# Kernel tuning notes

Measured on AMD Instinct MI355X. Metric: run time of the kernel, lower is better.

Reference implementation:

```python
import math
import jax, jax.numpy as jnp
import numpy as np

SEQ_LEN = 4096
PACK_LEN = 64
DIM = 1024
HEADS = 8
BS = 64
HD = DIM // HEADS
NB = SEQ_LEN // BS
PEN = -10000.0


def _slopes(n):
    start = 2.0 ** (-8.0 / n)
    return np.array([start ** (i + 1) for i in range(n)], dtype=np.float32)


def _dist_matrices():
    sl = _slopes(HEADS)
    idx = np.arange(SEQ_LEN, dtype=np.float32)
    D = sl[:, None, None] * np.abs(idx[:, None] - idx[None, :])  # [H,S,S]
    Dp = sl[:, None, None] * np.full((SEQ_LEN, PACK_LEN), float(BS), np.float32)  # [H,S,P]
    return jnp.asarray(D), jnp.asarray(Dp)


def _mb_index():
    # replicate get_middle_band_distances index construction (row counter from 0)
    M = (NB - 3) * BS
    i_vals = np.arange(2 * BS, SEQ_LEN - BS)
    offset = i_vals // BS - 1
    cols = np.concatenate([
        np.broadcast_to(np.arange(BS), (M, BS)),
        offset[:, None] * BS + np.arange(3 * BS)[None, :],
    ], axis=1)  # [M, 4*BS]
    rows = np.arange(M)
    return rows, cols

_MB_ROWS, _MB_COLS = _mb_index()


def _middle_band_D(D):
    return D[:, _MB_ROWS[:, None], _MB_COLS].reshape(HEADS, NB - 3, BS, 4 * BS)


def _heads(t):
    b, s, _ = t.shape
    return t.reshape(b, s, HEADS, HD).transpose(0, 2, 1, 3)


def reference(X, Cp, attention_mask, WQ, bQ, WK, bK, WV, bV):
    b, S, _ = X.shape
    rsq = 1.0 / math.sqrt(HD)
    D, Dp = _dist_matrices()

    q = _heads(X @ WQ + bQ)        # [b,H,S,hd]
    kx = _heads(X @ WK + bK)
    vx = _heads(X @ WV + bV)
    kcp = _heads(Cp @ WK + bK)     # [b,H,P,hd]
    vcp = _heads(Cp @ WV + bV)

    mask_block = attention_mask.reshape(b, NB, BS)
    exp_to = jnp.concatenate([mask_block[:, 1:-2], mask_block[:, 2:-1], mask_block[:, 3:]], axis=2)
    band_mask = jnp.einsum('blq,blk->blqk', mask_block[:, 2:-1], exp_to)[:, None]  # [b,1,L,bs,3bs]
    mask_v = attention_mask.reshape(b, 1, S, 1)

    # packed (Cp) attention path
    a = jnp.einsum('bhqd,bhkd->bhqk', q, kcp) * rsq - Dp[None] + (1.0 - mask_v) * PEN
    a = jax.nn.softmax(a, axis=-1)
    packed = jnp.einsum('bhqk,bhkd->bhqd', a, vcp) * mask_v  # [b,H,S,hd]

    qb = q.reshape(b, HEADS, NB, BS, HD)
    kb = kx.reshape(b, HEADS, NB, BS, HD)
    vb = vx.reshape(b, HEADS, NB, BS, HD)

    # first two rows attend to blocks 0..3
    k4 = kb[:, :, :4].reshape(b, HEADS, 4 * BS, HD)
    v4 = vb[:, :, :4].reshape(b, HEADS, 4 * BS, HD)
    q2 = qb[:, :, :2].reshape(b, HEADS, 2 * BS, HD)
    a1 = (jnp.einsum('bhqd,bhkd->bhqk', q2, k4) * rsq
          - D[:, :2 * BS, :4 * BS][None]
          + (1.0 - mask_v[:, :, :2 * BS, :1]) * PEN)
    a1 = jax.nn.softmax(a1, axis=-1)
    ctx_first = jnp.einsum('bhqk,bhkd->bhqd', a1, v4).reshape(b, HEADS, 2, BS, HD)

    # middle band: global block 0 + 3-block sliding window
    mk = jnp.concatenate([kb[:, :, 1:-2], kb[:, :, 2:-1], kb[:, :, 3:]], axis=3)  # [b,H,L,3bs,hd]
    mv = jnp.concatenate([vb[:, :, 1:-2], vb[:, :, 2:-1], vb[:, :, 3:]], axis=3)
    slid = jnp.einsum('bhlqd,bhlkd->bhlqk', qb[:, :, 2:-1], mk) + (1.0 - band_mask) * PEN
    glob = (jnp.einsum('bhlqd,bhkd->bhlqk', qb[:, :, 2:-1], kb[:, :, 0])
            + (1.0 - mask_block[:, 2:-1, :][..., None]) * PEN)  # torch-style broadcast (b==1)
    ma = jnp.concatenate([glob, slid], axis=-1) * rsq - _middle_band_D(D)[None]
    ma = jax.nn.softmax(ma, axis=-1)
    ctx_mid = (jnp.einsum('bhlqk,bhkd->bhlqd', ma[..., :BS], vb[:, :, 0])
               + jnp.einsum('bhlqk,bhlkd->bhlqd', ma[..., BS:], mv))

    # last row attends to blocks 0, -3, -2, -1 (no extra mask, as in original)
    kl = jnp.concatenate([kb[:, :, 0], kb[:, :, -3], kb[:, :, -2], kb[:, :, -1]], axis=2)
    vl = jnp.concatenate([vb[:, :, 0], vb[:, :, -3], vb[:, :, -2], vb[:, :, -1]], axis=2)
    al = jnp.einsum('bhqd,bhkd->bhqk', qb[:, :, -1], kl) * rsq - D[:, -BS:, -4 * BS:][None]
    al = jax.nn.softmax(al, axis=-1)
    ctx_last = jnp.einsum('bhqk,bhkd->bhqd', al, vl)[:, :, None]

    ctx = jnp.concatenate([ctx_first, ctx_mid, ctx_last], axis=2).reshape(b, HEADS, S, HD)
    # original does a raw view [b,h,S,hd] -> [b,S,h*hd] (no transpose); reshape matches
    Cx = (ctx + packed).reshape(b, S, HEADS * HD) * attention_mask[..., None]
    return Cx


def setup_inputs() -> dict:
    key = jax.random.key(0)
    ks = jax.random.split(key, 6)
    return {
        'X': jax.random.normal(ks[0], (1, SEQ_LEN, DIM), jnp.float32),
        'Cp': jax.random.normal(ks[1], (1, PACK_LEN, DIM), jnp.float32),
        'attention_mask': jnp.ones((1, SEQ_LEN), jnp.float32),
        'WQ': jax.random.normal(ks[2], (DIM, DIM), jnp.float32) * 0.02,
        'bQ': jnp.zeros((DIM,), jnp.float32),
        'WK': jax.random.normal(ks[3], (DIM, DIM), jnp.float32) * 0.02,
        'bK': jnp.zeros((DIM,), jnp.float32),
        'WV': jax.random.normal(ks[4], (DIM, DIM), jnp.float32) * 0.02,
        'bV': jnp.zeros((DIM,), jnp.float32),
    }
```

## Files before the change

### kernel.cpp

```cpp
#include <hip/hip_runtime.h>
#include <hip/hip_bf16.h>

typedef __bf16 bf16;
typedef __attribute__((ext_vector_type(4))) __bf16 bf16x4;
typedef __attribute__((ext_vector_type(8))) __bf16 bf16x8;
typedef __attribute__((ext_vector_type(4))) float f32x4;

#define SEQ   4096
#define DIMN  1024
#define NHEAD 8
#define HD    128
#define MALL  4160
#define PENV  -10000.0f
#define NT    16
#define NCVT  4160

typedef const __attribute__((address_space(1))) void gvoid_t;
typedef __attribute__((address_space(3))) void lvoid_t;

__global__ __launch_bounds__(256) void prep_kernel(
    const float* __restrict__ X, const float* __restrict__ Cp,
    const float* __restrict__ W0, const float* __restrict__ W1, const float* __restrict__ W2,
    bf16* __restrict__ A, bf16* __restrict__ Wt) {
  const int bid = blockIdx.x;
  if (bid < NCVT) {
    size_t base = ((size_t)bid * 256 + threadIdx.x) * 4;
    const float* src = (base < (size_t)SEQ * DIMN) ? (X + base) : (Cp + (base - (size_t)SEQ * DIMN));
    float4 v = *(const float4*)src;
    bf16x4 o;
    o[0] = (bf16)v.x; o[1] = (bf16)v.y; o[2] = (bf16)v.z; o[3] = (bf16)v.w;
    *(bf16x4*)&A[base] = o;
  } else {
    int tid2 = bid - NCVT;
    int z = tid2 >> 8, rem = tid2 & 255;
    int by = rem >> 4, bx = rem & 15;
    const float* W = (z == 0) ? W0 : ((z == 1) ? W1 : W2);
    bf16* dst = Wt + (size_t)z * DIMN * DIMN;
    __shared__ bf16 tile[64][72];
    int k0 = by * 64, n0 = bx * 64;
    int tx = threadIdx.x & 63, ty = threadIdx.x >> 6;
#pragma unroll
    for (int r = ty; r < 64; r += 4)
      tile[tx][r] = (bf16)W[(size_t)(k0 + r) * DIMN + n0 + tx];
    __syncthreads();
#pragma unroll
    for (int r = ty; r < 64; r += 4)
      dst[(size_t)(n0 + r) * DIMN + k0 + tx] = tile[r][tx];
  }
}

__global__ __launch_bounds__(512) void gemm_qkv_kernel(
    const bf16* __restrict__ A, const bf16* __restrict__ Wt,
    const float* __restrict__ bQ, const float* __restrict__ bK, const float* __restrict__ bV,
    bf16* __restrict__ QKV) {
  const int z = blockIdx.z;
  const int M = (z == 0) ? SEQ : MALL;
  const int m0 = blockIdx.y * 256;
  if (m0 >= M) return;
  const int n0 = blockIdx.x * 256;
  const bf16* Wz = Wt + (size_t)z * DIMN * DIMN;
  const float* bias = (z == 0) ? bQ : ((z == 1) ? bK : bV);
  bf16* out = QKV + (size_t)z * MALL * DIMN;

  __shared__ bf16 SMEM[4][256 * 64];
  bf16 (*Ab)[256 * 64] = &SMEM[0];
  bf16 (*Bb)[256 * 64] = &SMEM[2];

  const int t = threadIdx.x;
  const int lane = t & 63, w = t >> 6;
  const int wm = w >> 2, wn = w & 3;
  const int r16 = lane & 15, g4 = lane >> 4;

  f32x4 acc[8][4] = {};

  auto stageA = [&](int k) {
    int b = k & 1;
#pragma unroll
    for (int i = 0; i < 4; ++i) {
      int segBase = i * 512 + w * 64;
      int seg = segBase + lane;
      int row = seg >> 3;
      int cc = (seg & 7) ^ (row & 7);
      int gm = m0 + row; gm = (gm < M) ? gm : (M - 1);
      __builtin_amdgcn_global_load_lds(
          (gvoid_t*)(A + (size_t)gm * DIMN + k * 64 + cc * 8),
          (lvoid_t*)(&Ab[b][segBase * 8]), 16, 0, 0);
    }
  };
  auto stageB = [&](int k) {
    int b = k & 1;
#pragma unroll
    for (int i = 0; i < 4; ++i) {
      int segBase = i * 512 + w * 64;
      int seg = segBase + lane;
      int row = seg >> 3;
      int cc = (seg & 7) ^ (row & 7);
      int gn = n0 + row;
      __builtin_amdgcn_global_load_lds(
          (gvoid_t*)(Wz + (size_t)gn * DIMN + k * 64 + cc * 8),
          (lvoid_t*)(&Bb[b][segBase * 8]), 16, 0, 0);
    }
  };

  auto rdA = [&](const bf16* Ax, int mf, int kk) -> bf16x8 {
    int row = wm * 128 + mf * 16 + r16;
    return *(const bf16x8*)&Ax[row * 64 + (((kk * 4 + g4) ^ (row & 7)) * 8)];
  };
  auto rdB = [&](const bf16* Bx, int nf, int kk) -> bf16x8 {
    int row = wn * 64 + nf * 16 + r16;
    return *(const bf16x8*)&Bx[row * 64 + (((kk * 4 + g4) ^ (row & 7)) * 8)];
  };

  stageA(0); stageB(0);
  asm volatile("s_waitcnt vmcnt(0)" ::: "memory");
  __builtin_amdgcn_s_barrier();

  for (int k = 0; k < NT; ++k) {
    const bf16* Ax = &Ab[k & 1][0];
    const bf16* Bx = &Bb[k & 1][0];
    bf16x8 aL[4], aH[4], bL[4];

#pragma unroll
    for (int mf = 0; mf < 4; ++mf) aL[mf] = rdA(Ax, mf, 0);
#pragma unroll
    for (int nf = 0; nf < 4; ++nf) bL[nf] = rdB(Bx, nf, 0);
#pragma unroll
    for (int mf = 0; mf < 4; ++mf) aH[mf] = rdA(Ax, 4 + mf, 0);
    if (k + 1 < NT) stageA(k + 1);
    __builtin_amdgcn_sched_barrier(0);

    __builtin_amdgcn_s_setprio(1);
#pragma unroll
    for (int mf = 0; mf < 4; ++mf)
#pragma unroll
      for (int nf = 0; nf < 4; ++nf)
        acc[mf][nf] = __builtin_amdgcn_mfma_f32_16x16x32_bf16(aL[mf], bL[nf], acc[mf][nf], 0, 0, 0);
    __builtin_amdgcn_s_setprio(0);

    bf16x8 aL2[4], bL2[4];
#pragma unroll
    for (int mf = 0; mf < 4; ++mf) aL2[mf] = rdA(Ax, mf, 1);
#pragma unroll
    for (int nf = 0; nf < 4; ++nf) bL2[nf] = rdB(Bx, nf, 1);
    if (k + 1 < NT) stageB(k + 1);
    __builtin_amdgcn_sched_barrier(0);

    __builtin_amdgcn_s_setprio(1);
#pragma unroll
    for (int mf = 0; mf < 4; ++mf)
#pragma unroll
      for (int nf = 0; nf < 4; ++nf)
        acc[4 + mf][nf] = __builtin_amdgcn_mfma_f32_16x16x32_bf16(aH[mf], bL[nf], acc[4 + mf][nf], 0, 0, 0);
    __builtin_amdgcn_s_setprio(0);

#pragma unroll
    for (int mf = 0; mf < 4; ++mf) aH[mf] = rdA(Ax, 4 + mf, 1);

    __builtin_amdgcn_s_setprio(1);
#pragma unroll
    for (int mf = 0; mf < 4; ++mf)
#pragma unroll
      for (int nf = 0; nf < 4; ++nf)
        acc[mf][nf] = __builtin_amdgcn_mfma_f32_16x16x32_bf16(aL2[mf], bL2[nf], acc[mf][nf], 0, 0, 0);

#pragma unroll
    for (int mf = 0; mf < 4; ++mf)
#pragma unroll
      for (int nf = 0; nf < 4; ++nf)
        acc[4 + mf][nf] = __builtin_amdgcn_mfma_f32_16x16x32_bf16(aH[mf], bL2[nf], acc[4 + mf][nf], 0, 0, 0);
    __builtin_amdgcn_s_setprio(0);

    if (k + 1 < NT) {
      asm volatile("s_waitcnt vmcnt(0)" ::: "memory");
      __builtin_amdgcn_s_barrier();
    }
  }

  if (z == 2) {
    bf16* T = &SMEM[0][0];
    __syncthreads();
#pragma unroll
    for (int h = 0; h < 2; ++h) {
      if (wm == h) {
#pragma unroll
        for (int nf = 0; nf < 4; ++nf) {
          int n_loc = wn * 64 + nf * 16 + r16;
          float bv = bias[n0 + n_loc];
#pragma unroll
          for (int mf = 0; mf < 8; ++mf) {
            int m_rel = mf * 16 + g4 * 4;
            bf16x4 o;
#pragma unroll
            for (int r = 0; r < 4; ++r) o[r] = (bf16)(acc[mf][nf][r] + bv);
            *(bf16x4*)&T[n_loc * 132 + m_rel] = o;
          }
        }
      }
      __syncthreads();
#pragma unroll
      for (int it = 0; it < 8; ++it) {
        int n_loc = it * 32 + (t >> 4);
        int m8 = (t & 15) * 8;
        int gm = m0 + h * 128 + m8;
        if (gm < M) {
          bf16x8 v = *(const bf16x8*)&T[n_loc * 132 + m8];
          *(bf16x8*)&out[(size_t)(n0 + n_loc) * MALL + gm] = v;
        }
      }
      __syncthreads();
    }
  } else {
    bf16* T = &SMEM[0][0];
    __syncthreads();
#pragma unroll
    for (int h = 0; h < 2; ++h) {
      if (wm == h) {
#pragma unroll
        for (int nf = 0; nf < 4; ++nf) {
          int n_loc = wn * 64 + nf * 16 + r16;
          float bv = bias[n0 + n_loc];
#pragma unroll
          for (int mf = 0; mf < 8; ++mf) {
            int mb = mf * 16 + g4 * 4;
#pragma unroll
            for (int r = 0; r < 4; ++r)
              T[(mb + r) * 264 + n_loc] = (bf16)(acc[mf][nf][r] + bv);
          }
        }
      }
      __syncthreads();
#pragma unroll
      for (int it = 0; it < 8; ++it) {
        int m_rel = it * 16 + (t >> 5);
        int n8 = (t & 31) * 8;
        int gm = m0 + h * 128 + m_rel;
        if (gm < M) {
          bf16x8 v = *(const bf16x8*)&T[m_rel * 264 + n8];
          *(bf16x8*)&out[(size_t)gm * DIMN + n0 + n8] = v;
        }
      }
      __syncthreads();
    }
  }
}

__device__ __forceinline__ int key_row_map(int qb, int tslot) {
  if (qb <= 1) return tslot;
  if (qb == 63) return (tslot < 64) ? tslot : (3840 + tslot);
  return (tslot < 64) ? tslot : ((qb - 1) * 64 + (tslot - 64));
}

__global__ __launch_bounds__(256) void attn_kernel(
    const bf16* __restrict__ Q, const bf16* __restrict__ K, const bf16* __restrict__ VT,
    const float* __restrict__ mask, float* __restrict__ out) {
  const int bid = blockIdx.x;
  const int h = bid & 7, qb = bid >> 3;
  const int t = threadIdx.x;
  const int lane = t & 63, w = t >> 6;
  const int c16 = lane & 15, g4 = lane >> 4;
  const float sl = exp2f(-(float)(h + 1));
  const float rsq = 0.088388347648318447f;

  __shared__ bf16 KB[2][8192];
  __shared__ bf16 P[64][328];

  bf16x8 qf[4];
  {
    int srow = qb * 64 + w * 16 + c16;
    const bf16* qp = Q + (size_t)srow * DIMN + h * HD + g4 * 8;
#pragma unroll
    for (int ks = 0; ks < 4; ++ks) qf[ks] = *(const bf16x8*)(qp + ks * 32);
  }
  int iq[4]; float mi[4];
#pragma unroll
  for (int r = 0; r < 4; ++r) { iq[r] = qb * 64 + w * 16 + g4 * 4 + r; mi[r] = mask[iq[r]]; }
  float mjv[16];
#pragma unroll
  for (int f = 0; f < 16; ++f) mjv[f] = mask[key_row_map(qb, f * 16 + c16)];
  __builtin_amdgcn_sched_barrier(0);

  const bf16* vt_h = VT + (size_t)h * HD * MALL;

  auto stageC = [&](int c) {
    int b = c & 1;
    if (c < 5) {
#pragma unroll
      for (int i = 0; i < 4; ++i) {
        int segBase = i * 256 + w * 64;
        int seg = segBase + lane;
        int kr = seg >> 4;
        int cc = (seg & 15) ^ (kr & 7);
        int gr = (c == 4) ? (SEQ + kr) : key_row_map(qb, c * 64 + kr);
        __builtin_amdgcn_global_load_lds(
            (gvoid_t*)(K + (size_t)gr * DIMN + h * HD + cc * 8),
            (lvoid_t*)(&KB[b][segBase * 8]), 16, 0, 0);
      }
    } else {
      int j = c - 5;
      int colbase = (j == 4) ? SEQ : key_row_map(qb, j * 64);
#pragma unroll
      for (int i = 0; i < 4; ++i) {
        int segBase = i * 256 + w * 64;
        int seg = segBase + lane;
        int dr = seg >> 3;
        int cc = (seg & 7) ^ (dr & 7);
        __builtin_amdgcn_global_load_lds(
            (gvoid_t*)(vt_h + (size_t)dr * MALL + colbase + cc * 8),
            (lvoid_t*)(&KB[b][segBase * 8]), 16, 0, 0);
      }
    }
  };

  f32x4 sc[16] = {};
  f32x4 sp[4] = {};

  auto biasChunk = [&](int c) {
#pragma unroll
    for (int kj = 0; kj < 4; ++kj) {
      int f = c * 4 + kj;
      int tslot = f * 16 + c16;
      int jrow = key_row_map(qb, tslot);
      float mj = mjv[f];
      int jpos = (qb == 63) ? (3840 + tslot) : jrow;
      int ishift = (qb >= 2 && qb <= 62) ? 128 : 0;
#pragma unroll
      for (int r = 0; r < 4; ++r) {
        float raw = sc[f][r];
        float dist = sl * fabsf((float)(iq[r] - ishift - jpos));
        float s;
        if (qb <= 1)       s = raw * rsq - dist + (1.f - mi[r]) * PENV;
        else if (qb == 63) s = raw * rsq - dist;
        else {
          float pen = (tslot < 64) ? (1.f - mi[r]) * PENV : (1.f - mi[r] * mj) * PENV;
          s = (raw + pen) * rsq - dist;
        }
        sc[f][r] = s;
      }
    }
  };

  stageC(0);
#pragma unroll
  for (int c = 0; c < 5; ++c) {
    stageC(c + 1);
    if (c >= 1) biasChunk(c - 1);
    asm volatile("s_waitcnt vmcnt(4)" ::: "memory");
    __builtin_amdgcn_s_barrier();
    const bf16* Kx = &KB[c & 1][0];
    __builtin_amdgcn_s_setprio(1);
#pragma unroll
    for (int ks = 0; ks < 4; ++ks)
#pragma unroll
      for (int kj = 0; kj < 4; ++kj) {
        int row = kj * 16 + c16;
        bf16x8 bfr = *(const bf16x8*)&Kx[row * 128 + (((ks * 4 + g4) ^ (row & 7)) * 8)];
        if (c < 4)
          sc[c * 4 + kj] = __builtin_amdgcn_mfma_f32_16x16x32_bf16(qf[ks], bfr, sc[c * 4 + kj], 0, 0, 0);
        else
          sp[kj] = __builtin_amdgcn_mfma_f32_16x16x32_bf16(qf[ks], bfr, sp[kj], 0, 0, 0);
      }
    __builtin_amdgcn_s_setprio(0);
    __builtin_amdgcn_s_barrier();
  }

#pragma unroll
  for (int r = 0; r < 4; ++r) {
    float m = -1e30f;
#pragma unroll
    for (int f = 0; f < 16; ++f) m = fmaxf(m, sc[f][r]);
#pragma unroll
    for (int d = 1; d < 16; d <<= 1) m = fmaxf(m, __shfl_xor(m, d));
    float s = 0.f;
#pragma unroll
    for (int f = 0; f < 16; ++f) { float e = __expf(sc[f][r] - m); sc[f][r] = e; s += e; }
#pragma unroll
    for (int d = 1; d < 16; d <<= 1) s += __shfl_xor(s, d);
    float inv = 1.0f / s;
#pragma unroll
    for (int f = 0; f < 16; ++f)
      P[w * 16 + g4 * 4 + r][f * 16 + c16] = (bf16)(sc[f][r] * inv);
  }
#pragma unroll
  for (int r = 0; r < 4; ++r) {
    float m = -1e30f;
#pragma unroll
    for (int kj = 0; kj < 4; ++kj) m = fmaxf(m, sp[kj][r] * rsq);
#pragma unroll
    for (int d = 1; d < 16; d <<= 1) m = fmaxf(m, __shfl_xor(m, d));
    float s = 0.f;
    float e[4];
#pragma unroll
    for (int kj = 0; kj < 4; ++kj) { e[kj] = __expf(sp[kj][r] * rsq - m); s += e[kj]; }
#pragma unroll
    for (int d = 1; d < 16; d <<= 1) s += __shfl_xor(s, d);
    float inv = mi[r] / s;
#pragma unroll
    for (int kj = 0; kj < 4; ++kj)
      P[w * 16 + g4 * 4 + r][256 + kj * 16 + c16] = (bf16)(e[kj] * inv);
  }

  f32x4 ctx[8] = {};
#pragma unroll
  for (int j = 0; j < 5; ++j) {
    int c = j + 5;
    if (c < 9) {
      stageC(c + 1);
      asm volatile("s_waitcnt vmcnt(4)" ::: "memory");
    } else {
      asm volatile("s_waitcnt vmcnt(0)" ::: "memory");
    }
    __builtin_amdgcn_s_barrier();
    const bf16* Vx = &KB[c & 1][0];
    int pcol = (j < 4) ? j * 64 : 256;
    __builtin_amdgcn_s_setprio(1);
#pragma unroll
    for (int ks = 0; ks < 2; ++ks) {
      bf16x8 pa = *(const bf16x8*)&P[w * 16 + c16][pcol + ks * 32 + g4 * 8];
#pragma unroll
      for (int df = 0; df < 8; ++df) {
        int row = df * 16 + c16;
        bf16x8 bv = *(const bf16x8*)&Vx[row * 64 + (((ks * 4 + g4) ^ (row & 7)) * 8)];
        ctx[df] = __builtin_amdgcn_mfma_f32_16x16x32_bf16(pa, bv, ctx[df], 0, 0, 0);
      }
    }
    __builtin_amdgcn_s_setprio(0);
    __builtin_amdgcn_s_barrier();
  }

#pragma unroll
  for (int df = 0; df < 8; ++df) {
    int d = df * 16 + c16;
#pragma unroll
    for (int r = 0; r < 4; ++r) {
      int s = iq[r];
      float fm = mask[h * 512 + (s >> 3)];
      out[(size_t)h * (SEQ * HD) + (size_t)s * HD + d] = ctx[df][r] * fm;
    }
  }
}

extern "C" void kernel_launch(void* const* d_in, const int* in_sizes, int n_in,
                              void* d_out, int out_size, void* d_ws, size_t ws_size,
                              hipStream_t stream) {
  const float* X    = (const float*)d_in[0];
  const float* Cp   = (const float*)d_in[1];
  const float* mask = (const float*)d_in[2];
  const float* WQ   = (const float*)d_in[3];
  const float* bQ   = (const float*)d_in[4];
  const float* WK   = (const float*)d_in[5];
  const float* bK   = (const float*)d_in[6];
  const float* WV   = (const float*)d_in[7];
  const float* bV   = (const float*)d_in[8];
  float* out = (float*)d_out;

  bf16* Abf = (bf16*)d_ws;
  bf16* Wt  = Abf + (size_t)MALL * DIMN;
  bf16* QKV = Wt + (size_t)3 * DIMN * DIMN;

  prep_kernel<<<NCVT + 768, 256, 0, stream>>>(X, Cp, WQ, WK, WV, Abf, Wt);
  gemm_qkv_kernel<<<dim3(4, 17, 3), 512, 0, stream>>>(Abf, Wt, bQ, bK, bV, QKV);
  attn_kernel<<<512, 256, 0, stream>>>(QKV, QKV + (size_t)MALL * DIMN,
                                       QKV + (size_t)2 * MALL * DIMN, mask, out);
}
```

Before: 63.78 us.

## Shrink QKV GEMM tile to 256x128 with BK=32 and 4 waves

```diff
diff --git a/kernel.cpp b/kernel.cpp
--- a/kernel.cpp
+++ b/kernel.cpp
@@ -12,7 +12,7 @@
 #define HD    128
 #define MALL  4160
 #define PENV  -10000.0f
-#define NT    16
+#define NKT   32
 #define NCVT  4160
 
 typedef const __attribute__((address_space(1))) void gvoid_t;
@@ -49,7 +49,7 @@
   }
 }
 
-__global__ __launch_bounds__(512) void gemm_qkv_kernel(
+__global__ __launch_bounds__(256) void gemm_qkv_kernel(
     const bf16* __restrict__ A, const bf16* __restrict__ Wt,
     const float* __restrict__ bQ, const float* __restrict__ bK, const float* __restrict__ bV,
     bf16* __restrict__ QKV) {
@@ -57,189 +57,164 @@
   const int M = (z == 0) ? SEQ : MALL;
   const int m0 = blockIdx.y * 256;
   if (m0 >= M) return;
-  const int n0 = blockIdx.x * 256;
+  const int n0 = blockIdx.x * 128;
   const bf16* Wz = Wt + (size_t)z * DIMN * DIMN;
   const float* bias = (z == 0) ? bQ : ((z == 1) ? bK : bV);
   bf16* out = QKV + (size_t)z * MALL * DIMN;
 
-  __shared__ bf16 SMEM[4][256 * 64];
-  bf16 (*Ab)[256 * 64] = &SMEM[0];
-  bf16 (*Bb)[256 * 64] = &SMEM[2];
+  __shared__ bf16 SMEM[24576];
 
   const int t = threadIdx.x;
   const int lane = t & 63, w = t >> 6;
-  const int wm = w >> 2, wn = w & 3;
+  const int wm = w >> 1, wn = w & 1;
   const int r16 = lane & 15, g4 = lane >> 4;
 
   f32x4 acc[8][4] = {};
 
   auto stageA = [&](int k) {
-    int b = k & 1;
+    bf16* dst = SMEM + (k & 1) * 8192;
 #pragma unroll
     for (int i = 0; i < 4; ++i) {
-      int segBase = i * 512 + w * 64;
+      int segBase = (i * 4 + w) * 64;
       int seg = segBase + lane;
-      int row = seg >> 3;
-      int cc = (seg & 7) ^ (row & 7);
+      int row = seg >> 2;
+      int cc = (seg & 3) ^ ((row >> 1) & 3);
       int gm = m0 + row; gm = (gm < M) ? gm : (M - 1);
       __builtin_amdgcn_global_load_lds(
-          (gvoid_t*)(A + (size_t)gm * DIMN + k * 64 + cc * 8),
-          (lvoid_t*)(&Ab[b][segBase * 8]), 16, 0, 0);
+          (gvoid_t*)(A + (size_t)gm * DIMN + k * 32 + cc * 8),
+          (lvoid_t*)(dst + segBase * 8), 16, 0, 0);
     }
   };
   auto stageB = [&](int k) {
-    int b = k & 1;
-#pragma unroll
-    for (int i = 0; i < 4; ++i) {
-      int segBase = i * 512 + w * 64;
+    bf16* dst = SMEM + 16384 + (k & 1) * 4096;
+#pragma unroll
+    for (int i = 0; i < 2; ++i) {
+      int segBase = (i * 4 + w) * 64;
       int seg = segBase + lane;
-      int row = seg >> 3;
-      int cc = (seg & 7) ^ (row & 7);
+      int row = seg >> 2;
+      int cc = (seg & 3) ^ ((row >> 1) & 3);
       int gn = n0 + row;
       __builtin_amdgcn_global_load_lds(
-          (gvoid_t*)(Wz + (size_t)gn * DIMN + k * 64 + cc * 8),
-          (lvoid_t*)(&Bb[b][segBase * 8]), 16, 0, 0);
-    }
-  };
-
-  auto rdA = [&](const bf16* Ax, int mf, int kk) -> bf16x8 {
+          (gvoid_t*)(Wz + (size_t)gn * DIMN + k * 32 + cc * 8),
+          (lvoid_t*)(dst + segBase * 8), 16, 0, 0);
+    }
+  };
+
+  auto rdA = [&](const bf16* Ax, int mf) -> bf16x8 {
     int row = wm * 128 + mf * 16 + r16;
-    return *(const bf16x8*)&Ax[row * 64 + (((kk * 4 + g4) ^ (row & 7)) * 8)];
-  };
-  auto rdB = [&](const bf16* Bx, int nf, int kk) -> bf16x8 {
+    return *(const bf16x8*)&Ax[row * 32 + ((g4 ^ ((row >> 1) & 3)) * 8)];
+  };
+  auto rdB = [&](const bf16* Bx, int nf) -> bf16x8 {
     int row = wn * 64 + nf * 16 + r16;
-    return *(const bf16x8*)&Bx[row * 64 + (((kk * 4 + g4) ^ (row & 7)) * 8)];
+    return *(const bf16x8*)&Bx[row * 32 + ((g4 ^ ((row >> 1) & 3)) * 8)];
   };
 
   stageA(0); stageB(0);
   asm volatile("s_waitcnt vmcnt(0)" ::: "memory");
   __builtin_amdgcn_s_barrier();
 
-  for (int k = 0; k < NT; ++k) {
-    const bf16* Ax = &Ab[k & 1][0];
-    const bf16* Bx = &Bb[k & 1][0];
-    bf16x8 aL[4], aH[4], bL[4];
-
-#pragma unroll
-    for (int mf = 0; mf < 4; ++mf) aL[mf] = rdA(Ax, mf, 0);
-#pragma unroll
-    for (int nf = 0; nf < 4; ++nf) bL[nf] = rdB(Bx, nf, 0);
-#pragma unroll
-    for (int mf = 0; mf < 4; ++mf) aH[mf] = rdA(Ax, 4 + mf, 0);
-    if (k + 1 < NT) stageA(k + 1);
+  for (int k = 0; k < NKT; ++k) {
+    const bf16* Ax = SMEM + (k & 1) * 8192;
+    const bf16* Bx = SMEM + 16384 + (k & 1) * 4096;
+    bf16x8 aL[4], aH[4], bF[4];
+
+#pragma unroll
+    for (int mf = 0; mf < 4; ++mf) aL[mf] = rdA(Ax, mf);
+#pragma unroll
+    for (int nf = 0; nf < 4; ++nf) bF[nf] = rdB(Bx, nf);
+    if (k + 1 < NKT) stageA(k + 1);
     __builtin_amdgcn_sched_barrier(0);
-
     __builtin_amdgcn_s_setprio(1);
 #pragma unroll
     for (int mf = 0; mf < 4; ++mf)
 #pragma unroll
       for (int nf = 0; nf < 4; ++nf)
-        acc[mf][nf] = __builtin_amdgcn_mfma_f32_16x16x32_bf16(aL[mf], bL[nf], acc[mf][nf], 0, 0, 0);
+        acc[mf][nf] = __builtin_amdgcn_mfma_f32_16x16x32_bf16(aL[mf], bF[nf], acc[mf][nf], 0, 0, 0);
     __builtin_amdgcn_s_setprio(0);
 
-    bf16x8 aL2[4], bL2[4];
-#pragma unroll
-    for (int mf = 0; mf < 4; ++mf) aL2[mf] = rdA(Ax, mf, 1);
-#pragma unroll
-    for (int nf = 0; nf < 4; ++nf) bL2[nf] = rdB(Bx, nf, 1);
-    if (k + 1 < NT) stageB(k + 1);
+#pragma unroll
+    for (int mf = 0; mf < 4; ++mf) aH[mf] = rdA(Ax, 4 + mf);
+    if (k + 1 < NKT) stageB(k + 1);
     __builtin_amdgcn_sched_barrier(0);
-
     __builtin_amdgcn_s_setprio(1);
 #pragma unroll
     for (int mf = 0; mf < 4; ++mf)
 #pragma unroll
       for (int nf = 0; nf < 4; ++nf)
-        acc[4 + mf][nf] = __builtin_amdgcn_mfma_f32_16x16x32_bf16(aH[mf], bL[nf], acc[4 + mf][nf], 0, 0, 0);
+        acc[4 + mf][nf] = __builtin_amdgcn_mfma_f32_16x16x32_bf16(aH[mf], bF[nf], acc[4 + mf][nf], 0, 0, 0);
     __builtin_amdgcn_s_setprio(0);
 
-#pragma unroll
-    for (int mf = 0; mf < 4; ++mf) aH[mf] = rdA(Ax, 4 + mf, 1);
-
-    __builtin_amdgcn_s_setprio(1);
-#pragma unroll
-    for (int mf = 0; mf < 4; ++mf)
-#pragma unroll
-      for (int nf = 0; nf < 4; ++nf)
-        acc[mf][nf] = __builtin_amdgcn_mfma_f32_16x16x32_bf16(aL2[mf], bL2[nf], acc[mf][nf], 0, 0, 0);
-
-#pragma unroll
-    for (int mf = 0; mf < 4; ++mf)
-#pragma unroll
-      for (int nf = 0; nf < 4; ++nf)
-        acc[4 + mf][nf] = __builtin_amdgcn_mfma_f32_16x16x32_bf16(aH[mf], bL2[nf], acc[4 + mf][nf], 0, 0, 0);
-    __builtin_amdgcn_s_setprio(0);
-
-    if (k + 1 < NT) {
+    if (k + 1 < NKT) {
       asm volatile("s_waitcnt vmcnt(0)" ::: "memory");
       __builtin_amdgcn_s_barrier();
     }
   }
 
+  __syncthreads();
   if (z == 2) {
-    bf16* T = &SMEM[0][0];
-    __syncthreads();
-#pragma unroll
-    for (int h = 0; h < 2; ++h) {
-      if (wm == h) {
-#pragma unroll
-        for (int nf = 0; nf < 4; ++nf) {
-          int n_loc = wn * 64 + nf * 16 + r16;
-          float bv = bias[n0 + n_loc];
-#pragma unroll
-          for (int mf = 0; mf < 8; ++mf) {
-            int m_rel = mf * 16 + g4 * 4;
-            bf16x4 o;
-#pragma unroll
-            for (int r = 0; r < 4; ++r) o[r] = (bf16)(acc[mf][nf][r] + bv);
-            *(bf16x4*)&T[n_loc * 132 + m_rel] = o;
+    bf16* T = SMEM;
+#pragma unroll
+    for (int q = 0; q < 4; ++q) {
+      if ((m0 + q * 64) < M) {
+        if (wm == (q >> 1)) {
+#pragma unroll
+          for (int nf = 0; nf < 4; ++nf) {
+            int n_loc = wn * 64 + nf * 16 + r16;
+            float bv = bias[n0 + n_loc];
+#pragma unroll
+            for (int mfq = 0; mfq < 4; ++mfq) {
+              int mf = (q & 1) * 4 + mfq;
+              bf16x4 o;
+#pragma unroll
+              for (int r = 0; r < 4; ++r) o[r] = (bf16)(acc[mf][nf][r] + bv);
+              *(bf16x4*)&T[n_loc * 66 + mfq * 16 + g4 * 4] = o;
+            }
           }
         }
-      }
-      __syncthreads();
-#pragma unroll
-      for (int it = 0; it < 8; ++it) {
-        int n_loc = it * 32 + (t >> 4);
-        int m8 = (t & 15) * 8;
-        int gm = m0 + h * 128 + m8;
-        if (gm < M) {
-          bf16x8 v = *(const bf16x8*)&T[n_loc * 132 + m8];
-          *(bf16x8*)&out[(size_t)(n0 + n_loc) * MALL + gm] = v;
+        __syncthreads();
+#pragma unroll
+        for (int it = 0; it < 4; ++it) {
+          int idx = it * 256 + t;
+          int n_loc = idx >> 3, m8 = (idx & 7) * 8;
+          bf16x8 v = *(const bf16x8*)&T[n_loc * 66 + m8];
+          *(bf16x8*)&out[(size_t)(n0 + n_loc) * MALL + m0 + q * 64 + m8] = v;
         }
-      }
-      __syncthreads();
+        __syncthreads();
+      }
     }
   } else {
-    bf16* T = &SMEM[0][0];
-    __syncthreads();
-#pragma unroll
-    for (int h = 0; h < 2; ++h) {
-      if (wm == h) {
-#pragma unroll
-        for (int nf = 0; nf < 4; ++nf) {
-          int n_loc = wn * 64 + nf * 16 + r16;
-          float bv = bias[n0 + n_loc];
-#pragma unroll
-          for (int mf = 0; mf < 8; ++mf) {
-            int mb = mf * 16 + g4 * 4;
-#pragma unroll
-            for (int r = 0; r < 4; ++r)
-              T[(mb + r) * 264 + n_loc] = (bf16)(acc[mf][nf][r] + bv);
+    bf16* T = SMEM;
+#pragma unroll
+    for (int q = 0; q < 4; ++q) {
+      if ((m0 + q * 64) < M) {
+        if (wm == (q >> 1)) {
+#pragma unroll
+          for (int nf = 0; nf < 4; ++nf) {
+            int n_loc = wn * 64 + nf * 16 + r16;
+            float bv = bias[n0 + n_loc];
+#pragma unroll
+            for (int mfq = 0; mfq < 4; ++mfq) {
+              int mf = (q & 1) * 4 + mfq;
+              int mb = mfq * 16 + g4 * 4;
+#pragma unroll
+              for (int r = 0; r < 4; ++r)
+                T[(mb + r) * 264 + n_loc] = (bf16)(acc[mf][nf][r] + bv);
+            }
           }
         }
-      }
-      __syncthreads();
-#pragma unroll
-      for (int it = 0; it < 8; ++it) {
-        int m_rel = it * 16 + (t >> 5);
-        int n8 = (t & 31) * 8;
-        int gm = m0 + h * 128 + m_rel;
-        if (gm < M) {
-          bf16x8 v = *(const bf16x8*)&T[m_rel * 264 + n8];
-          *(bf16x8*)&out[(size_t)gm * DIMN + n0 + n8] = v;
+        __syncthreads();
+#pragma unroll
+        for (int it = 0; it < 4; ++it) {
+          int idx = it * 256 + t;
+          int m_rel = idx >> 4, n8 = (idx & 15) * 8;
+          int gm = m0 + q * 64 + m_rel;
+          if (gm < M) {
+            bf16x8 v = *(const bf16x8*)&T[m_rel * 264 + n8];
+            *(bf16x8*)&out[(size_t)gm * DIMN + n0 + n8] = v;
+          }
         }
-      }
-      __syncthreads();
+        __syncthreads();
+      }
     }
   }
 }
@@ -458,7 +433,7 @@
   bf16* QKV = Wt + (size_t)3 * DIMN * DIMN;
 
   prep_kernel<<<NCVT + 768, 256, 0, stream>>>(X, Cp, WQ, WK, WV, Abf, Wt);
-  gemm_qkv_kernel<<<dim3(4, 17, 3), 512, 0, stream>>>(Abf, Wt, bQ, bK, bV, QKV);
+  gemm_qkv_kernel<<<dim3(8, 17, 3), 256, 0, stream>>>(Abf, Wt, bQ, bK, bV, QKV);
   attn_kernel<<<512, 256, 0, stream>>>(QKV, QKV + (size_t)MALL * DIMN,
                                        QKV + (size_t)2 * MALL * DIMN, mask, out);
 }
```

Result: slower. 105.1 us (+64.8%).
